# Optimization experiments

Measured on AMD Instinct MI355X. Metric: run time of the kernel, lower is better.

The kernel has to match this reference:

```python
import jax, jax.numpy as jnp
import numpy as np


def setup_inputs() -> dict:
    key = jax.random.key(0)
    ks = jax.random.split(key, 5)
    B, S, H, E, F = 2, 2048, 2048, 8, 2048
    return {
        "hidden_states": jax.random.normal(ks[0], (B, S, H), dtype=jnp.float32),
        "gate_w": jax.random.normal(ks[1], (E, H), dtype=jnp.float32) * 0.02,
        "w1s": jax.random.normal(ks[2], (E, H, F), dtype=jnp.float32) * 0.02,
        "w2s": jax.random.normal(ks[3], (E, F, H), dtype=jnp.float32) * 0.02,
        "w3s": jax.random.normal(ks[4], (E, H, F), dtype=jnp.float32) * 0.02,
        "top_k": 2,
    }


def reference(hidden_states, gate_w, w1s, w2s, w3s, top_k):
    B, S, H = hidden_states.shape
    E = gate_w.shape[0]
    x = hidden_states.reshape(-1, H)               # [T, H]
    T = x.shape[0]
    # Router: softmax in fp32, top-k, renormalize (matches torch F.softmax(dtype=float))
    logits = x @ gate_w.T                          # [T, E]
    probs = jax.nn.softmax(logits.astype(jnp.float32), axis=-1)
    topw, topi = jax.lax.top_k(probs, top_k)       # [T, k]
    topw = topw / jnp.sum(topw, axis=-1, keepdims=True)
    # Dense combine weights [T, E]: zero for unselected experts.
    combine = jnp.zeros((T, E), dtype=x.dtype)
    combine = combine.at[jnp.arange(T)[:, None], topi].add(topw.astype(x.dtype))
    # Expert FFN (SwiGLU): silu(x @ w1) * (x @ w3) @ w2, per expert.
    h1 = jnp.einsum("th,ehf->etf", x, w1s)         # [E, T, F]
    h3 = jnp.einsum("th,ehf->etf", x, w3s)
    h = jax.nn.silu(h1) * h3
    out_e = jnp.einsum("etf,efh->eth", h, w2s)      # [E, T, H]
    out = jnp.einsum("eth,te->th", out_e, combine)  # weighted merge
    return out.reshape(B, S, H)
```

## Files before the change

kernel.cpp:

```cpp
#include <hip/hip_runtime.h>
#include <cstdint>
#include <cstddef>

#define Tt 4096
#define Hd 2048
#define Fd 2048
#define En 8
#define Rcap 9216

typedef short bf16x8 __attribute__((ext_vector_type(8)));
typedef float f32x4 __attribute__((ext_vector_type(4)));
typedef unsigned int u32;
typedef u32 __attribute__((address_space(1))) gas_u32;
typedef u32 __attribute__((address_space(3))) las_u32;

__device__ __forceinline__ unsigned short f2bf(float f) {
    u32 u = __builtin_bit_cast(u32, f);
    u = (u + 0x7FFFu + ((u >> 16) & 1u)) >> 16;
    return (unsigned short)u;
}
__device__ __forceinline__ float bf2f(unsigned short s) {
    return __builtin_bit_cast(float, ((u32)s) << 16);
}

__global__ __launch_bounds__(256) void router_kernel(
    const float* __restrict__ x, const float* __restrict__ gate,
    int* __restrict__ topi, float* __restrict__ topw)
{
    const int t = blockIdx.x;
    const float* xr = x + (size_t)t * Hd;
    float acc[En];
    #pragma unroll
    for (int e = 0; e < En; ++e) acc[e] = 0.f;
    for (int h = threadIdx.x; h < Hd; h += 256) {
        const float xv = xr[h];
        #pragma unroll
        for (int e = 0; e < En; ++e) acc[e] += xv * gate[e * Hd + h];
    }
    #pragma unroll
    for (int e = 0; e < En; ++e) {
        float v = acc[e];
        for (int d = 32; d > 0; d >>= 1) v += __shfl_down(v, d, 64);
        acc[e] = v;
    }
    __shared__ float red[En][4];
    const int lane = threadIdx.x & 63, wv = threadIdx.x >> 6;
    if (lane == 0) {
        #pragma unroll
        for (int e = 0; e < En; ++e) red[e][wv] = acc[e];
    }
    __syncthreads();
    if (threadIdx.x == 0) {
        float l[En];
        #pragma unroll
        for (int e = 0; e < En; ++e) l[e] = red[e][0] + red[e][1] + red[e][2] + red[e][3];
        float m = l[0];
        #pragma unroll
        for (int e = 1; e < En; ++e) m = fmaxf(m, l[e]);
        float p[En];
        #pragma unroll
        for (int e = 0; e < En; ++e) p[e] = expf(l[e] - m);
        int i1 = 0;
        #pragma unroll
        for (int e = 1; e < En; ++e) if (p[e] > p[i1]) i1 = e;
        int i2 = (i1 == 0) ? 1 : 0;
        #pragma unroll
        for (int e = 0; e < En; ++e) if (e != i1 && p[e] > p[i2]) i2 = e;
        const float s = p[i1] + p[i2];
        topi[2 * t] = i1; topi[2 * t + 1] = i2;
        topw[2 * t] = p[i1] / s; topw[2 * t + 1] = p[i2] / s;
    }
}

__global__ void assign_kernel(const int* __restrict__ topi, int* __restrict__ cnt,
                              int* __restrict__ posbuf)
{
    const int idx = blockIdx.x * blockDim.x + threadIdx.x;
    if (idx >= Tt * 2) return;
    posbuf[idx] = atomicAdd(&cnt[topi[idx]], 1);
}

__global__ void scan_kernel(const int* __restrict__ cnt, int* __restrict__ off,
                            int* __restrict__ pcnt)
{
    if (threadIdx.x == 0 && blockIdx.x == 0) {
        int a = 0;
        for (int e = 0; e < En; ++e) {
            off[e] = a;
            const int pc = (cnt[e] + 127) & ~127;
            pcnt[e] = pc;
            a += pc;
        }
    }
}

__global__ __launch_bounds__(256) void gather_kernel(
    const float* __restrict__ x, const int* __restrict__ topi,
    const float* __restrict__ topw, const int* __restrict__ off,
    const int* __restrict__ posbuf, unsigned short* __restrict__ Xg,
    int* __restrict__ tokrow, float* __restrict__ wrow)
{
    const int entry = blockIdx.x;
    const int t = entry >> 1;
    const int e = topi[entry];
    const int row = off[e] + posbuf[entry];
    if (threadIdx.x == 0) { tokrow[row] = t; wrow[row] = topw[entry]; }
    const float4* src = (const float4*)(x + (size_t)t * Hd);
    const int i = threadIdx.x;
    const float4 a = src[2 * i], b = src[2 * i + 1];
    unsigned short o[8];
    o[0] = f2bf(a.x); o[1] = f2bf(a.y); o[2] = f2bf(a.z); o[3] = f2bf(a.w);
    o[4] = f2bf(b.x); o[5] = f2bf(b.y); o[6] = f2bf(b.z); o[7] = f2bf(b.w);
    ((uint4*)(Xg + (size_t)row * Hd))[i] = *(const uint4*)o;
}

__global__ __launch_bounds__(256) void transpose_kernel(
    const float* __restrict__ w1s, const float* __restrict__ w3s,
    const float* __restrict__ w2s, unsigned short* __restrict__ w1T,
    unsigned short* __restrict__ w3T, unsigned short* __restrict__ w2T)
{
    __shared__ float tile[32][33];
    const int z = blockIdx.z, tensor = z >> 3, e = z & 7;
    const float* src = (tensor == 0) ? w1s : (tensor == 1) ? w3s : w2s;
    unsigned short* dst = (tensor == 0) ? w1T : (tensor == 1) ? w3T : w2T;
    const int c0 = blockIdx.x * 32, r0 = blockIdx.y * 32;
    const int tx = threadIdx.x & 31, ty = threadIdx.x >> 5;
    const size_t base = (size_t)e * 2048 * 2048;
    #pragma unroll
    for (int r = 0; r < 4; ++r)
        tile[ty + r * 8][tx] = src[base + (size_t)(r0 + ty + r * 8) * 2048 + c0 + tx];
    __syncthreads();
    #pragma unroll
    for (int r = 0; r < 4; ++r)
        dst[base + (size_t)(c0 + ty + r * 8) * 2048 + r0 + tx] = f2bf(tile[tx][ty + r * 8]);
}

template <int EPI>
__global__ __launch_bounds__(256) void gemm_kernel(
    const unsigned short* __restrict__ Ab,
    const unsigned short* __restrict__ Bb0,
    const unsigned short* __restrict__ Bb1,
    unsigned short* __restrict__ C0,
    unsigned short* __restrict__ C1,
    float* __restrict__ outp,
    const int* __restrict__ off, const int* __restrict__ pcnt,
    const int* __restrict__ tokrow, const float* __restrict__ wrow)
{
    const int z = blockIdx.z;
    const int e = (EPI == 0) ? (z >> 1) : z;
    const int mt = blockIdx.y;
    const int pc = pcnt[e];
    if (mt * 128 >= pc) return;
    const int nt = blockIdx.x;
    const int row0 = off[e] + mt * 128;

    const unsigned short* A = Ab + (size_t)row0 * 2048;
    const unsigned short* Bsel = (EPI == 0 && (z & 1)) ? Bb1 : Bb0;
    const unsigned short* B = Bsel + (size_t)e * 2048 * 2048 + (size_t)nt * 128 * 2048;

    __shared__ __align__(16) unsigned short As[128 * 64];
    __shared__ __align__(16) unsigned short Bs[128 * 64];

    const int tid = threadIdx.x;
    const int lane = tid & 63;
    const int wv = tid >> 6;
    const int wm = wv & 1, wn = wv >> 1;
    const int quad = lane >> 4, l16 = lane & 15;

    f32x4 acc[4][4];
    const f32x4 zero4 = {0.f, 0.f, 0.f, 0.f};
    #pragma unroll
    for (int i = 0; i < 4; ++i)
        #pragma unroll
        for (int j = 0; j < 4; ++j) acc[i][j] = zero4;

    for (int kt = 0; kt < 2048; kt += 64) {
        __syncthreads();
        #pragma unroll
        for (int i = 0; i < 4; ++i) {
            const int grp = i * 4 + wv;
            const int idx = grp * 64 + lane;
            const int r = idx >> 3;
            const int kc = (idx & 7) ^ (r & 7);
            const unsigned short* ga = A + (size_t)r * 2048 + kt + kc * 8;
            __builtin_amdgcn_global_load_lds((const gas_u32*)ga,
                                             (las_u32*)(As + grp * 512), 16, 0, 0);
            const unsigned short* gb = B + (size_t)r * 2048 + kt + kc * 8;
            __builtin_amdgcn_global_load_lds((const gas_u32*)gb,
                                             (las_u32*)(Bs + grp * 512), 16, 0, 0);
        }
        __syncthreads();
        #pragma unroll
        for (int ks = 0; ks < 2; ++ks) {
            bf16x8 af[4], bfr[4];
            #pragma unroll
            for (int mi = 0; mi < 4; ++mi) {
                const int m = wm * 64 + mi * 16 + l16;
                const int ck = ks * 4 + quad;
                const int slot = m * 8 + (ck ^ (m & 7));
                af[mi] = *(const bf16x8*)(As + slot * 8);
            }
            #pragma unroll
            for (int ni = 0; ni < 4; ++ni) {
                const int n = wn * 64 + ni * 16 + l16;
                const int ck = ks * 4 + quad;
                const int slot = n * 8 + (ck ^ (n & 7));
                bfr[ni] = *(const bf16x8*)(Bs + slot * 8);
            }
            #pragma unroll
            for (int mi = 0; mi < 4; ++mi)
                #pragma unroll
                for (int ni = 0; ni < 4; ++ni)
                    acc[mi][ni] = __builtin_amdgcn_mfma_f32_16x16x32_bf16(
                        af[mi], bfr[ni], acc[mi][ni], 0, 0, 0);
        }
    }

    if (EPI == 0) {
        unsigned short* C = (z & 1) ? C1 : C0;
        #pragma unroll
        for (int mi = 0; mi < 4; ++mi) {
            const int rbase = row0 + wm * 64 + mi * 16 + quad * 4;
            #pragma unroll
            for (int ni = 0; ni < 4; ++ni) {
                const int col = nt * 128 + wn * 64 + ni * 16 + l16;
                #pragma unroll
                for (int r = 0; r < 4; ++r)
                    C[(size_t)(rbase + r) * 2048 + col] = f2bf(acc[mi][ni][r]);
            }
        }
    } else {
        #pragma unroll
        for (int mi = 0; mi < 4; ++mi) {
            const int rbase = row0 + wm * 64 + mi * 16 + quad * 4;
            #pragma unroll
            for (int r = 0; r < 4; ++r) {
                const int rg = rbase + r;
                const int t = tokrow[rg];
                const float w = wrow[rg];
                float* orow = outp + (size_t)t * 2048 + nt * 128 + wn * 64;
                #pragma unroll
                for (int ni = 0; ni < 4; ++ni)
                    unsafeAtomicAdd(orow + ni * 16 + l16, acc[mi][ni][r] * w);
            }
        }
    }
}

__global__ __launch_bounds__(256) void silumul_kernel(
    unsigned short* __restrict__ H1buf, const unsigned short* __restrict__ H3buf)
{
    const size_t idx = ((size_t)blockIdx.x * 256 + threadIdx.x) * 8;
    uint4 h1 = *(const uint4*)(H1buf + idx);
    const uint4 h3 = *(const uint4*)(H3buf + idx);
    unsigned short* p1 = (unsigned short*)&h1;
    const unsigned short* p3 = (const unsigned short*)&h3;
    #pragma unroll
    for (int j = 0; j < 8; ++j) {
        const float a = bf2f(p1[j]);
        const float b = bf2f(p3[j]);
        const float s = a / (1.f + expf(-a));
        p1[j] = f2bf(s * b);
    }
    *(uint4*)(H1buf + idx) = h1;
}

static constexpr size_t SZ_WT  = (size_t)En * 2048 * 2048 * 2;
static constexpr size_t SZ_XG  = (size_t)Rcap * 2048 * 2;
static constexpr size_t O_W1T  = 0;
static constexpr size_t O_W3T  = O_W1T + SZ_WT;
static constexpr size_t O_W2T  = O_W3T + SZ_WT;
static constexpr size_t O_XG   = O_W2T + SZ_WT;
static constexpr size_t O_H1   = O_XG + SZ_XG;
static constexpr size_t O_H3   = O_H1 + SZ_XG;
static constexpr size_t O_TOPI = O_H3 + SZ_XG;
static constexpr size_t O_TOPW = O_TOPI + (size_t)Tt * 2 * 4;
static constexpr size_t O_POS  = O_TOPW + (size_t)Tt * 2 * 4;
static constexpr size_t O_OFF  = O_POS + (size_t)Tt * 2 * 4;
static constexpr size_t O_PCNT = O_OFF + 64;
static constexpr size_t O_CNT  = O_PCNT + 64;
static constexpr size_t O_TOKROW = O_CNT + 64;
static constexpr size_t O_WROW = O_TOKROW + (size_t)Rcap * 4;
static constexpr size_t ZERO_SZ = 64 + (size_t)Rcap * 4 + (size_t)Rcap * 4;

extern "C" void kernel_launch(void* const* d_in, const int* in_sizes, int n_in,
                              void* d_out, int out_size, void* d_ws, size_t ws_size,
                              hipStream_t stream)
{
    const float* x    = (const float*)d_in[0];
    const float* gate = (const float*)d_in[1];
    const float* w1s  = (const float*)d_in[2];
    const float* w2s  = (const float*)d_in[3];
    const float* w3s  = (const float*)d_in[4];
    float* out = (float*)d_out;
    char* ws = (char*)d_ws;

    unsigned short* w1T = (unsigned short*)(ws + O_W1T);
    unsigned short* w3T = (unsigned short*)(ws + O_W3T);
    unsigned short* w2T = (unsigned short*)(ws + O_W2T);
    unsigned short* Xg  = (unsigned short*)(ws + O_XG);
    unsigned short* H1  = (unsigned short*)(ws + O_H1);
    unsigned short* H3  = (unsigned short*)(ws + O_H3);
    int*   topi   = (int*)(ws + O_TOPI);
    float* topw   = (float*)(ws + O_TOPW);
    int*   posbuf = (int*)(ws + O_POS);
    int*   off    = (int*)(ws + O_OFF);
    int*   pcnt   = (int*)(ws + O_PCNT);
    int*   cnt    = (int*)(ws + O_CNT);
    int*   tokrow = (int*)(ws + O_TOKROW);
    float* wrow   = (float*)(ws + O_WROW);

    hipMemsetAsync(out, 0, (size_t)Tt * Hd * 4, stream);
    hipMemsetAsync(ws + O_XG, 0, SZ_XG, stream);
    hipMemsetAsync(ws + O_CNT, 0, ZERO_SZ, stream);

    transpose_kernel<<<dim3(64, 64, 24), 256, 0, stream>>>(w1s, w3s, w2s, w1T, w3T, w2T);
    router_kernel<<<Tt, 256, 0, stream>>>(x, gate, topi, topw);
    assign_kernel<<<(Tt * 2) / 256, 256, 0, stream>>>(topi, cnt, posbuf);
    scan_kernel<<<1, 64, 0, stream>>>(cnt, off, pcnt);
    gather_kernel<<<Tt * 2, 256, 0, stream>>>(x, topi, topw, off, posbuf, Xg, tokrow, wrow);

    gemm_kernel<0><<<dim3(16, 32, 16), 256, 0, stream>>>(
        Xg, w1T, w3T, H1, H3, nullptr, off, pcnt, tokrow, wrow);
    silumul_kernel<<<(Rcap * Fd) / 2048, 256, 0, stream>>>(H1, H3);
    gemm_kernel<1><<<dim3(16, 32, 8), 256, 0, stream>>>(
        H1, w2T, nullptr, nullptr, nullptr, out, off, pcnt, tokrow, wrow);
}
```

Baseline: 873.0 us.

## Fuse SwiGLU into gate/up GEMM, replace atomic scatter with combine kernel

The gate and up projections now run in one GEMM kernel, with different waves computing w1 and w3 tiles and SiLU-multiply applied in the epilogue. This removes the separate silumul pass and the H1/H3 round trips. The down projection writes weighted bf16 rows, and a separate combine kernel sums each token's two rows, replacing float atomics and the output memset. The router also does the expert-slot atomics, removing the assign kernel, and the weight transpose uses 64x64 tiles with vectorized loads and stores. The trade-offs are extra bf16 rounding of the per-expert outputs before the sum and an additional intermediate buffer.

Result: slower. 916.4 us (+5.0%).

```diff
diff --git a/kernel.cpp b/kernel.cpp
--- a/kernel.cpp
+++ b/kernel.cpp
@@ -25,7 +25,8 @@
 
 __global__ __launch_bounds__(256) void router_kernel(
     const float* __restrict__ x, const float* __restrict__ gate,
-    int* __restrict__ topi, float* __restrict__ topw)
+    int* __restrict__ topi, float* __restrict__ topw,
+    int* __restrict__ cnt, int* __restrict__ posbuf)
 {
     const int t = blockIdx.x;
     const float* xr = x + (size_t)t * Hd;
@@ -69,15 +70,9 @@
         const float s = p[i1] + p[i2];
         topi[2 * t] = i1; topi[2 * t + 1] = i2;
         topw[2 * t] = p[i1] / s; topw[2 * t + 1] = p[i2] / s;
-    }
-}
-
-__global__ void assign_kernel(const int* __restrict__ topi, int* __restrict__ cnt,
-                              int* __restrict__ posbuf)
-{
-    const int idx = blockIdx.x * blockDim.x + threadIdx.x;
-    if (idx >= Tt * 2) return;
-    posbuf[idx] = atomicAdd(&cnt[topi[idx]], 1);
+        posbuf[2 * t]     = atomicAdd(&cnt[i1], 1);
+        posbuf[2 * t + 1] = atomicAdd(&cnt[i2], 1);
+    }
 }
 
 __global__ void scan_kernel(const int* __restrict__ cnt, int* __restrict__ off,
@@ -98,13 +93,13 @@
     const float* __restrict__ x, const int* __restrict__ topi,
     const float* __restrict__ topw, const int* __restrict__ off,
     const int* __restrict__ posbuf, unsigned short* __restrict__ Xg,
-    int* __restrict__ tokrow, float* __restrict__ wrow)
+    int* __restrict__ rowof, float* __restrict__ wrow)
 {
     const int entry = blockIdx.x;
     const int t = entry >> 1;
     const int e = topi[entry];
     const int row = off[e] + posbuf[entry];
-    if (threadIdx.x == 0) { tokrow[row] = t; wrow[row] = topw[entry]; }
+    if (threadIdx.x == 0) { rowof[entry] = row; wrow[row] = topw[entry]; }
     const float4* src = (const float4*)(x + (size_t)t * Hd);
     const int i = threadIdx.x;
     const float4 a = src[2 * i], b = src[2 * i + 1];
@@ -119,44 +114,172 @@
     const float* __restrict__ w2s, unsigned short* __restrict__ w1T,
     unsigned short* __restrict__ w3T, unsigned short* __restrict__ w2T)
 {
-    __shared__ float tile[32][33];
+    __shared__ float tile[64][65];
     const int z = blockIdx.z, tensor = z >> 3, e = z & 7;
     const float* src = (tensor == 0) ? w1s : (tensor == 1) ? w3s : w2s;
     unsigned short* dst = (tensor == 0) ? w1T : (tensor == 1) ? w3T : w2T;
-    const int c0 = blockIdx.x * 32, r0 = blockIdx.y * 32;
-    const int tx = threadIdx.x & 31, ty = threadIdx.x >> 5;
+    const int c0 = blockIdx.x * 64, r0 = blockIdx.y * 64;
     const size_t base = (size_t)e * 2048 * 2048;
-    #pragma unroll
-    for (int r = 0; r < 4; ++r)
-        tile[ty + r * 8][tx] = src[base + (size_t)(r0 + ty + r * 8) * 2048 + c0 + tx];
+    const int tid = threadIdx.x;
+    const int ltx = tid & 15, lty = tid >> 4;
+    #pragma unroll
+    for (int p = 0; p < 4; ++p) {
+        const int rr = lty + p * 16;
+        const float4 v = *(const float4*)(src + base + (size_t)(r0 + rr) * 2048 + c0 + ltx * 4);
+        tile[rr][ltx * 4 + 0] = v.x;
+        tile[rr][ltx * 4 + 1] = v.y;
+        tile[rr][ltx * 4 + 2] = v.z;
+        tile[rr][ltx * 4 + 3] = v.w;
+    }
     __syncthreads();
-    #pragma unroll
-    for (int r = 0; r < 4; ++r)
-        dst[base + (size_t)(c0 + ty + r * 8) * 2048 + r0 + tx] = f2bf(tile[tx][ty + r * 8]);
-}
-
-template <int EPI>
-__global__ __launch_bounds__(256) void gemm_kernel(
-    const unsigned short* __restrict__ Ab,
-    const unsigned short* __restrict__ Bb0,
-    const unsigned short* __restrict__ Bb1,
-    unsigned short* __restrict__ C0,
-    unsigned short* __restrict__ C1,
-    float* __restrict__ outp,
-    const int* __restrict__ off, const int* __restrict__ pcnt,
-    const int* __restrict__ tokrow, const float* __restrict__ wrow)
-{
-    const int z = blockIdx.z;
-    const int e = (EPI == 0) ? (z >> 1) : z;
+    const int rx = tid & 7, cy = tid >> 3;
+    #pragma unroll
+    for (int p = 0; p < 2; ++p) {
+        const int cc = cy + p * 32;
+        unsigned short o[8];
+        #pragma unroll
+        for (int j = 0; j < 8; ++j) o[j] = f2bf(tile[rx * 8 + j][cc]);
+        *(uint4*)(dst + base + (size_t)(c0 + cc) * 2048 + r0 + rx * 8) = *(const uint4*)o;
+    }
+}
+
+__global__ __launch_bounds__(256) void gemm13_kernel(
+    const unsigned short* __restrict__ Xg,
+    const unsigned short* __restrict__ w1T,
+    const unsigned short* __restrict__ w3T,
+    unsigned short* __restrict__ G,
+    const int* __restrict__ off, const int* __restrict__ pcnt)
+{
+    const int e = blockIdx.z;
     const int mt = blockIdx.y;
     const int pc = pcnt[e];
     if (mt * 128 >= pc) return;
     const int nt = blockIdx.x;
     const int row0 = off[e] + mt * 128;
 
-    const unsigned short* A = Ab + (size_t)row0 * 2048;
-    const unsigned short* Bsel = (EPI == 0 && (z & 1)) ? Bb1 : Bb0;
-    const unsigned short* B = Bsel + (size_t)e * 2048 * 2048 + (size_t)nt * 128 * 2048;
+    const unsigned short* A  = Xg + (size_t)row0 * 2048;
+    const unsigned short* B1 = w1T + (size_t)e * 2048 * 2048 + (size_t)nt * 64 * 2048;
+    const unsigned short* B3 = w3T + (size_t)e * 2048 * 2048 + (size_t)nt * 64 * 2048;
+
+    __shared__ __align__(16) unsigned short As[128 * 64];
+    __shared__ __align__(16) unsigned short Bs1[64 * 64];
+    __shared__ __align__(16) unsigned short Bs3[64 * 64];
+
+    const int tid = threadIdx.x;
+    const int lane = tid & 63;
+    const int wv = tid >> 6;
+    const int wm = wv & 1, wt = wv >> 1;
+    const int quad = lane >> 4, l16 = lane & 15;
+    const unsigned short* BsW = (wt == 0) ? Bs1 : Bs3;
+
+    f32x4 acc[4][4];
+    const f32x4 zero4 = {0.f, 0.f, 0.f, 0.f};
+    #pragma unroll
+    for (int i = 0; i < 4; ++i)
+        #pragma unroll
+        for (int j = 0; j < 4; ++j) acc[i][j] = zero4;
+
+    for (int kt = 0; kt < 2048; kt += 64) {
+        __syncthreads();
+        #pragma unroll
+        for (int i = 0; i < 4; ++i) {
+            const int grp = i * 4 + wv;
+            const int idx = grp * 64 + lane;
+            const int r = idx >> 3;
+            const int kc = (idx & 7) ^ (r & 7);
+            __builtin_amdgcn_global_load_lds(
+                (const gas_u32*)(A + (size_t)r * 2048 + kt + kc * 8),
+                (las_u32*)(As + (size_t)grp * 512), 16, 0, 0);
+        }
+        #pragma unroll
+        for (int i = 0; i < 2; ++i) {
+            const int grp = i * 4 + wv;
+            const int idx = grp * 64 + lane;
+            const int r = idx >> 3;
+            const int kc = (idx & 7) ^ (r & 7);
+            __builtin_amdgcn_global_load_lds(
+                (const gas_u32*)(B1 + (size_t)r * 2048 + kt + kc * 8),
+                (las_u32*)(Bs1 + (size_t)grp * 512), 16, 0, 0);
+            __builtin_amdgcn_global_load_lds(
+                (const gas_u32*)(B3 + (size_t)r * 2048 + kt + kc * 8),
+                (las_u32*)(Bs3 + (size_t)grp * 512), 16, 0, 0);
+        }
+        __syncthreads();
+        #pragma unroll
+        for (int ks = 0; ks < 2; ++ks) {
+            const int ck = ks * 4 + quad;
+            bf16x8 af[4], bfr[4];
+            #pragma unroll
+            for (int mi = 0; mi < 4; ++mi) {
+                const int m = wm * 64 + mi * 16 + l16;
+                af[mi] = *(const bf16x8*)(As + (m * 8 + (ck ^ (m & 7))) * 8);
+            }
+            #pragma unroll
+            for (int ni = 0; ni < 4; ++ni) {
+                const int n = ni * 16 + l16;
+                bfr[ni] = *(const bf16x8*)(BsW + (n * 8 + (ck ^ (n & 7))) * 8);
+            }
+            #pragma unroll
+            for (int mi = 0; mi < 4; ++mi)
+                #pragma unroll
+                for (int ni = 0; ni < 4; ++ni)
+                    acc[mi][ni] = __builtin_amdgcn_mfma_f32_16x16x32_bf16(
+                        af[mi], bfr[ni], acc[mi][ni], 0, 0, 0);
+        }
+    }
+
+    __syncthreads();
+    unsigned short* Gx = As;
+    if (wt == 1) {
+        #pragma unroll
+        for (int mi = 0; mi < 4; ++mi) {
+            const int rb = wm * 64 + mi * 16 + quad * 4;
+            #pragma unroll
+            for (int ni = 0; ni < 4; ++ni) {
+                const int col = ni * 16 + l16;
+                #pragma unroll
+                for (int r = 0; r < 4; ++r)
+                    Gx[(rb + r) * 64 + col] = f2bf(acc[mi][ni][r]);
+            }
+        }
+    }
+    __syncthreads();
+    if (wt == 0) {
+        #pragma unroll
+        for (int mi = 0; mi < 4; ++mi) {
+            const int rb = wm * 64 + mi * 16 + quad * 4;
+            #pragma unroll
+            for (int ni = 0; ni < 4; ++ni) {
+                const int col = ni * 16 + l16;
+                const int gcol = nt * 64 + col;
+                #pragma unroll
+                for (int r = 0; r < 4; ++r) {
+                    const float h1 = acc[mi][ni][r];
+                    const float h3 = bf2f(Gx[(rb + r) * 64 + col]);
+                    const float s = h1 / (1.f + expf(-h1));
+                    G[(size_t)(row0 + rb + r) * 2048 + gcol] = f2bf(s * h3);
+                }
+            }
+        }
+    }
+}
+
+__global__ __launch_bounds__(256) void gemm2_kernel(
+    const unsigned short* __restrict__ G,
+    const unsigned short* __restrict__ w2T,
+    unsigned short* __restrict__ OR,
+    const int* __restrict__ off, const int* __restrict__ pcnt,
+    const float* __restrict__ wrow)
+{
+    const int e = blockIdx.z;
+    const int mt = blockIdx.y;
+    const int pc = pcnt[e];
+    if (mt * 128 >= pc) return;
+    const int nt = blockIdx.x;
+    const int row0 = off[e] + mt * 128;
+
+    const unsigned short* A = G + (size_t)row0 * 2048;
+    const unsigned short* B = w2T + (size_t)e * 2048 * 2048 + (size_t)nt * 128 * 2048;
 
     __shared__ __align__(16) unsigned short As[128 * 64];
     __shared__ __align__(16) unsigned short Bs[128 * 64];
@@ -182,30 +305,27 @@
             const int idx = grp * 64 + lane;
             const int r = idx >> 3;
             const int kc = (idx & 7) ^ (r & 7);
-            const unsigned short* ga = A + (size_t)r * 2048 + kt + kc * 8;
-            __builtin_amdgcn_global_load_lds((const gas_u32*)ga,
-                                             (las_u32*)(As + grp * 512), 16, 0, 0);
-            const unsigned short* gb = B + (size_t)r * 2048 + kt + kc * 8;
-            __builtin_amdgcn_global_load_lds((const gas_u32*)gb,
-                                             (las_u32*)(Bs + grp * 512), 16, 0, 0);
+            __builtin_amdgcn_global_load_lds(
+                (const gas_u32*)(A + (size_t)r * 2048 + kt + kc * 8),
+                (las_u32*)(As + (size_t)grp * 512), 16, 0, 0);
+            __builtin_amdgcn_global_load_lds(
+                (const gas_u32*)(B + (size_t)r * 2048 + kt + kc * 8),
+                (las_u32*)(Bs + (size_t)grp * 512), 16, 0, 0);
         }
         __syncthreads();
         #pragma unroll
         for (int ks = 0; ks < 2; ++ks) {
+            const int ck = ks * 4 + quad;
             bf16x8 af[4], bfr[4];
             #pragma unroll
             for (int mi = 0; mi < 4; ++mi) {
                 const int m = wm * 64 + mi * 16 + l16;
-                const int ck = ks * 4 + quad;
-                const int slot = m * 8 + (ck ^ (m & 7));
-                af[mi] = *(const bf16x8*)(As + slot * 8);
+                af[mi] = *(const bf16x8*)(As + (m * 8 + (ck ^ (m & 7))) * 8);
             }
             #pragma unroll
             for (int ni = 0; ni < 4; ++ni) {
                 const int n = wn * 64 + ni * 16 + l16;
-                const int ck = ks * 4 + quad;
-                const int slot = n * 8 + (ck ^ (n & 7));
-                bfr[ni] = *(const bf16x8*)(Bs + slot * 8);
+                bfr[ni] = *(const bf16x8*)(Bs + (n * 8 + (ck ^ (n & 7))) * 8);
             }
             #pragma unroll
             for (int mi = 0; mi < 4; ++mi)
@@ -216,72 +336,58 @@
         }
     }
 
-    if (EPI == 0) {
-        unsigned short* C = (z & 1) ? C1 : C0;
-        #pragma unroll
-        for (int mi = 0; mi < 4; ++mi) {
-            const int rbase = row0 + wm * 64 + mi * 16 + quad * 4;
+    #pragma unroll
+    for (int mi = 0; mi < 4; ++mi) {
+        const int rbase = row0 + wm * 64 + mi * 16 + quad * 4;
+        #pragma unroll
+        for (int r = 0; r < 4; ++r) {
+            const int rg = rbase + r;
+            const float w = wrow[rg];
             #pragma unroll
             for (int ni = 0; ni < 4; ++ni) {
                 const int col = nt * 128 + wn * 64 + ni * 16 + l16;
-                #pragma unroll
-                for (int r = 0; r < 4; ++r)
-                    C[(size_t)(rbase + r) * 2048 + col] = f2bf(acc[mi][ni][r]);
-            }
-        }
-    } else {
-        #pragma unroll
-        for (int mi = 0; mi < 4; ++mi) {
-            const int rbase = row0 + wm * 64 + mi * 16 + quad * 4;
-            #pragma unroll
-            for (int r = 0; r < 4; ++r) {
-                const int rg = rbase + r;
-                const int t = tokrow[rg];
-                const float w = wrow[rg];
-                float* orow = outp + (size_t)t * 2048 + nt * 128 + wn * 64;
-                #pragma unroll
-                for (int ni = 0; ni < 4; ++ni)
-                    unsafeAtomicAdd(orow + ni * 16 + l16, acc[mi][ni][r] * w);
-            }
-        }
-    }
-}
-
-__global__ __launch_bounds__(256) void silumul_kernel(
-    unsigned short* __restrict__ H1buf, const unsigned short* __restrict__ H3buf)
-{
-    const size_t idx = ((size_t)blockIdx.x * 256 + threadIdx.x) * 8;
-    uint4 h1 = *(const uint4*)(H1buf + idx);
-    const uint4 h3 = *(const uint4*)(H3buf + idx);
-    unsigned short* p1 = (unsigned short*)&h1;
-    const unsigned short* p3 = (const unsigned short*)&h3;
-    #pragma unroll
-    for (int j = 0; j < 8; ++j) {
-        const float a = bf2f(p1[j]);
-        const float b = bf2f(p3[j]);
-        const float s = a / (1.f + expf(-a));
-        p1[j] = f2bf(s * b);
-    }
-    *(uint4*)(H1buf + idx) = h1;
+                OR[(size_t)rg * 2048 + col] = f2bf(acc[mi][ni][r] * w);
+            }
+        }
+    }
+}
+
+__global__ __launch_bounds__(256) void combine_kernel(
+    const unsigned short* __restrict__ OR, const int* __restrict__ rowof,
+    float* __restrict__ out)
+{
+    const int t = blockIdx.x;
+    const int r0 = rowof[2 * t], r1 = rowof[2 * t + 1];
+    const int j = threadIdx.x;
+    const uint4 a = *(const uint4*)(OR + (size_t)r0 * 2048 + j * 8);
+    const uint4 b = *(const uint4*)(OR + (size_t)r1 * 2048 + j * 8);
+    const unsigned short* pa = (const unsigned short*)&a;
+    const unsigned short* pb = (const unsigned short*)&b;
+    float o[8];
+    #pragma unroll
+    for (int k = 0; k < 8; ++k) o[k] = bf2f(pa[k]) + bf2f(pb[k]);
+    float* dst = out + (size_t)t * 2048 + j * 8;
+    *(float4*)dst = *(const float4*)o;
+    *(float4*)(dst + 4) = *(const float4*)(o + 4);
 }
 
 static constexpr size_t SZ_WT  = (size_t)En * 2048 * 2048 * 2;
-static constexpr size_t SZ_XG  = (size_t)Rcap * 2048 * 2;
+static constexpr size_t SZ_RB  = (size_t)Rcap * 2048 * 2;
 static constexpr size_t O_W1T  = 0;
 static constexpr size_t O_W3T  = O_W1T + SZ_WT;
 static constexpr size_t O_W2T  = O_W3T + SZ_WT;
 static constexpr size_t O_XG   = O_W2T + SZ_WT;
-static constexpr size_t O_H1   = O_XG + SZ_XG;
-static constexpr size_t O_H3   = O_H1 + SZ_XG;
-static constexpr size_t O_TOPI = O_H3 + SZ_XG;
+static constexpr size_t O_G    = O_XG + SZ_RB;
+static constexpr size_t O_OR   = O_G + SZ_RB;
+static constexpr size_t O_TOPI = O_OR + SZ_RB;
 static constexpr size_t O_TOPW = O_TOPI + (size_t)Tt * 2 * 4;
 static constexpr size_t O_POS  = O_TOPW + (size_t)Tt * 2 * 4;
-static constexpr size_t O_OFF  = O_POS + (size_t)Tt * 2 * 4;
+static constexpr size_t O_ROW  = O_POS + (size_t)Tt * 2 * 4;
+static constexpr size_t O_OFF  = O_ROW + (size_t)Tt * 2 * 4;
 static constexpr size_t O_PCNT = O_OFF + 64;
 static constexpr size_t O_CNT  = O_PCNT + 64;
-static constexpr size_t O_TOKROW = O_CNT + 64;
-static constexpr size_t O_WROW = O_TOKROW + (size_t)Rcap * 4;
-static constexpr size_t ZERO_SZ = 64 + (size_t)Rcap * 4 + (size_t)Rcap * 4;
+static constexpr size_t O_WROW = O_CNT + 64;
+static constexpr size_t ZERO_SZ = 64 + (size_t)Rcap * 4;
 
 extern "C" void kernel_launch(void* const* d_in, const int* in_sizes, int n_in,
                               void* d_out, int out_size, void* d_ws, size_t ws_size,
@@ -299,30 +405,26 @@
     unsigned short* w3T = (unsigned short*)(ws + O_W3T);
     unsigned short* w2T = (unsigned short*)(ws + O_W2T);
     unsigned short* Xg  = (unsigned short*)(ws + O_XG);
-    unsigned short* H1  = (unsigned short*)(ws + O_H1);
-    unsigned short* H3  = (unsigned short*)(ws + O_H3);
+    unsigned short* G   = (unsigned short*)(ws + O_G);
+    unsigned short* OR  = (unsigned short*)(ws + O_OR);
     int*   topi   = (int*)(ws + O_TOPI);
     float* topw   = (float*)(ws + O_TOPW);
     int*   posbuf = (int*)(ws + O_POS);
+    int*   rowof  = (int*)(ws + O_ROW);
     int*   off    = (int*)(ws + O_OFF);
     int*   pcnt   = (int*)(ws + O_PCNT);
     int*   cnt    = (int*)(ws + O_CNT);
-    int*   tokrow = (int*)(ws + O_TOKROW);
     float* wrow   = (float*)(ws + O_WROW);
 
-    hipMemsetAsync(out, 0, (size_t)Tt * Hd * 4, stream);
-    hipMemsetAsync(ws + O_XG, 0, SZ_XG, stream);
+    hipMemsetAsync(ws + O_XG, 0, SZ_RB, stream);
     hipMemsetAsync(ws + O_CNT, 0, ZERO_SZ, stream);
 
-    transpose_kernel<<<dim3(64, 64, 24), 256, 0, stream>>>(w1s, w3s, w2s, w1T, w3T, w2T);
-    router_kernel<<<Tt, 256, 0, stream>>>(x, gate, topi, topw);
-    assign_kernel<<<(Tt * 2) / 256, 256, 0, stream>>>(topi, cnt, posbuf);
+    transpose_kernel<<<dim3(32, 32, 24), 256, 0, stream>>>(w1s, w3s, w2s, w1T, w3T, w2T);
+    router_kernel<<<Tt, 256, 0, stream>>>(x, gate, topi, topw, cnt, posbuf);
     scan_kernel<<<1, 64, 0, stream>>>(cnt, off, pcnt);
-    gather_kernel<<<Tt * 2, 256, 0, stream>>>(x, topi, topw, off, posbuf, Xg, tokrow, wrow);
-
-    gemm_kernel<0><<<dim3(16, 32, 16), 256, 0, stream>>>(
-        Xg, w1T, w3T, H1, H3, nullptr, off, pcnt, tokrow, wrow);
-    silumul_kernel<<<(Rcap * Fd) / 2048, 256, 0, stream>>>(H1, H3);
-    gemm_kernel<1><<<dim3(16, 32, 8), 256, 0, stream>>>(
-        H1, w2T, nullptr, nullptr, nullptr, out, off, pcnt, tokrow, wrow);
-}
+    gather_kernel<<<Tt * 2, 256, 0, stream>>>(x, topi, topw, off, posbuf, Xg, rowof, wrow);
+
+    gemm13_kernel<<<dim3(32, 32, 8), 256, 0, stream>>>(Xg, w1T, w3T, G, off, pcnt);
+    gemm2_kernel<<<dim3(16, 32, 8), 256, 0, stream>>>(G, w2T, OR, off, pcnt, wrow);
+    combine_kernel<<<Tt, 256, 0, stream>>>(OR, rowof, out);
+}
```
